# Kernel optimization log

Hardware: AMD Instinct MI355X
Metric: run time of the kernel (lower is better)

Reference implementation:

```python
import jax, jax.numpy as jnp
import numpy as np

B, T, EMB, H = 8, 1024, 128, 8


def setup_inputs() -> dict:
    key = jax.random.key(0)
    ks = jax.random.split(key, 7)
    s = 0.02
    return {
        "x": jax.random.normal(ks[0], (B, T, EMB), dtype=jnp.float32),
        "mask": jax.random.randint(ks[1], (1, T, T), 0, 2, dtype=jnp.int32),
        "Wk": (jax.random.normal(ks[2], (EMB * H, EMB), dtype=jnp.float32) * s),
        "Wq": (jax.random.normal(ks[3], (EMB * H, EMB), dtype=jnp.float32) * s),
        "Wv": (jax.random.normal(ks[4], (EMB * H, EMB), dtype=jnp.float32) * s),
        "Wu": (jax.random.normal(ks[5], (EMB, EMB * H), dtype=jnp.float32) * s),
        "bu": (jax.random.normal(ks[6], (EMB,), dtype=jnp.float32) * s),
    }


def reference(x, mask, Wk, Wq, Wv, Wu, bu):
    b, t, e = x.shape  # e == emb; per-head dim also == emb in this module
    h = Wk.shape[0] // e
    # projections: (b,t,e) @ (e, h*e) -> (b,t,h,e) -> (b,h,t,e)
    q = (x @ Wq.T).reshape(b, t, h, e).transpose(0, 2, 1, 3)
    k = (x @ Wk.T).reshape(b, t, h, e).transpose(0, 2, 1, 3)
    v = (x @ Wv.T).reshape(b, t, h, e).transpose(0, 2, 1, 3)
    scale = e ** 0.25  # torch scales q and k each by e**(1/4)
    dot = jnp.einsum('bhqe,bhke->bhqk', q / scale, k / scale)
    # causal mask: strictly-upper triangle (offset=1) set to -inf FIRST
    causal = jnp.triu(jnp.ones((t, t), dtype=bool), k=1)
    dot = jnp.where(causal, -jnp.inf, dot)
    # padding mask: where mask==0 set to -1e9 (overwrites -inf where overlapping)
    dot = jnp.where(mask[:, None] == 0, jnp.float32(-1e9), dot)
    attn = jax.nn.softmax(dot, axis=-1)
    out = jnp.einsum('bhqk,bhke->bhqe', attn, v)
    out = out.transpose(0, 2, 1, 3).reshape(b, t, h * e)
    return out @ Wu.T + bu
```

## Files before the change

### kernel.cpp

```cpp
#include <hip/hip_runtime.h>

#define Bn 8
#define Hn 8
#define Tn 1024
#define Dn 128

typedef __attribute__((ext_vector_type(8))) short bf16x8;
typedef __attribute__((ext_vector_type(4))) float f32x4;

typedef __attribute__((address_space(3))) unsigned int lds_as_t;
typedef __attribute__((address_space(1))) const unsigned int glb_as_t;

static __device__ __forceinline__ void gload_lds16(const unsigned short* g, unsigned short* l) {
    __builtin_amdgcn_global_load_lds((glb_as_t*)g, (lds_as_t*)l, 16, 0, 0);
}
static __device__ __forceinline__ void gload_lds16b(const char* g, char* l) {
    __builtin_amdgcn_global_load_lds((glb_as_t*)g, (lds_as_t*)l, 16, 0, 0);
}

static __device__ __forceinline__ unsigned short f2bf(float f) {
    union { float f; unsigned int u; } v; v.f = f;
    unsigned int u = v.u;
    return (unsigned short)((u + 0x7FFFu + ((u >> 16) & 1u)) >> 16);
}
static __device__ __forceinline__ int pack_bf16_trunc(float lo, float hi) {
    union { float f; unsigned int u; } a, b;
    a.f = lo; b.f = hi;
    return (int)__builtin_amdgcn_perm(b.u, a.u, 0x07060302u);
}

__global__ __launch_bounds__(256) void prep_kernel(
    const float* __restrict__ x,  const float* __restrict__ Wq,
    const float* __restrict__ Wk, const float* __restrict__ Wv,
    const float* __restrict__ Wu, const int* __restrict__ mask,
    const float* __restrict__ bu, float* __restrict__ outp,
    unsigned short* __restrict__ xb,  unsigned short* __restrict__ wqB,
    unsigned short* __restrict__ wkB, unsigned short* __restrict__ wvB,
    unsigned short* __restrict__ wuF, unsigned long long* __restrict__ bits)
{
    const int blk = blockIdx.x;
    const int tid = threadIdx.x;

    if (blk < 1408) {
        const float* in; unsigned short* out; int i4;
        if (blk < 1024)      { in = x;  out = xb;  i4 = blk * 256 + tid; }
        else if (blk < 1152) { in = Wq; out = wqB; i4 = (blk - 1024) * 256 + tid; }
        else if (blk < 1280) { in = Wk; out = wkB; i4 = (blk - 1152) * 256 + tid; }
        else                 { in = Wv; out = wvB; i4 = (blk - 1280) * 256 + tid; }
        float4 f = ((const float4*)in)[i4];
        ushort4 o;
        o.x = f2bf(f.x); o.y = f2bf(f.y); o.z = f2bf(f.z); o.w = f2bf(f.w);
        int base = i4 * 4;
        int row = base >> 7, col = base & 127;
        int scol = (((col >> 3) ^ (row & 15)) << 3) | (col & 7);
        *(ushort4*)(out + row * 128 + scol) = o;
    } else if (blk < 1536) {
        if (tid < 128) {
            int id = (blk - 1408) * 128 + tid;
            int lane_ = id & 63;
            int fid = id >> 6;
            int nt = fid & 7, ks = (fid >> 3) & 3, h = fid >> 5;
            int row = nt * 16 + (lane_ & 15);
            int col = h * 128 + ks * 32 + (lane_ >> 4) * 8;
            const float* src = Wu + (size_t)row * 1024 + col;
            float4 f0 = *(const float4*)(src);
            float4 f1 = *(const float4*)(src + 4);
            unsigned short o[8];
            o[0] = f2bf(f0.x); o[1] = f2bf(f0.y); o[2] = f2bf(f0.z); o[3] = f2bf(f0.w);
            o[4] = f2bf(f1.x); o[5] = f2bf(f1.y); o[6] = f2bf(f1.z); o[7] = f2bf(f1.w);
            *(ushort4*)(wuF + (size_t)id * 8)     = *(ushort4*)&o[0];
            *(ushort4*)(wuF + (size_t)id * 8 + 4) = *(ushort4*)&o[4];
        }
    } else if (blk < 2560) {
        int wid  = (blk - 1536) * 4 + (tid >> 6);
        int lane = tid & 63;
#pragma unroll
        for (int i = 0; i < 4; i++) {
            int widx = wid * 4 + i;
            int row = widx >> 4, kt = widx & 15;
            int v = mask[row * Tn + kt * 64 + lane];
            unsigned long long b = __ballot(v != 0);
            if (lane == 0) bits[kt * Tn + row] = b;
        }
    } else {
        int f4 = (blk - 2560) * 1024 + tid * 4;
#pragma unroll
        for (int i = 0; i < 4; i++)
            ((float4*)outp)[f4 + i] = ((const float4*)bu)[(f4 + i) & 31];
    }
}

__global__ __launch_bounds__(256, 1) void qkv_kernel(
    const unsigned short* __restrict__ xb,
    const unsigned short* __restrict__ wqB,
    const unsigned short* __restrict__ wkB,
    const unsigned short* __restrict__ wvB,
    char* __restrict__ Q,
    char* __restrict__ K,
    unsigned short* __restrict__ Vt)
{
    const int bx = blockIdx.x, by = blockIdx.y;
    const int wave = threadIdx.x >> 6;
    const int lane = threadIdx.x & 63;
    const int l16  = lane & 15;
    const int quad = lane >> 4;
    const int wm = wave & 1, wn = wave >> 1;

    __shared__ __align__(16) unsigned short As[128 * 128];
    __shared__ __align__(16) unsigned short Bs[3][128 * 128];
    __shared__ __align__(16) char escr[128 * 144];

    const unsigned short* Ag = xb + (size_t)bx * 128 * 128;
    const unsigned short* Bg0 = wqB + (size_t)by * 128 * 128;
    const unsigned short* Bg1 = wkB + (size_t)by * 128 * 128;
    const unsigned short* Bg2 = wvB + (size_t)by * 128 * 128;

#pragma unroll
    for (int i = 0; i < 8; i++) {
        int base = (wave * 8 + i) * 512;
        gload_lds16(Ag  + base + lane * 8, &As[base]);
        gload_lds16(Bg0 + base + lane * 8, &Bs[0][base]);
    }
    __syncthreads();

    bf16x8 a[4][4];
#pragma unroll
    for (int mt = 0; mt < 4; mt++) {
        int row = wm * 64 + mt * 16 + l16;
#pragma unroll
        for (int ks = 0; ks < 4; ks++)
            a[mt][ks] = *(const bf16x8*)(&As[row * 128 + (((ks * 4 + quad) ^ (row & 15)) << 3)]);
    }

    const int h_ = by;
    const int b_ = bx >> 3;
    f32x4 acc[4][4];

    {
#pragma unroll
        for (int i = 0; i < 8; i++) {
            int base = (wave * 8 + i) * 512;
            gload_lds16(Bg1 + base + lane * 8, &Bs[1][base]);
        }
#pragma unroll
        for (int nt = 0; nt < 4; nt++) {
            int row = wn * 64 + nt * 16 + l16;
            bf16x8 b4[4];
#pragma unroll
            for (int ks = 0; ks < 4; ks++)
                b4[ks] = *(const bf16x8*)(&Bs[0][row * 128 + (((ks * 4 + quad) ^ (row & 15)) << 3)]);
#pragma unroll
            for (int mt = 0; mt < 4; mt++) {
                f32x4 c = {0.f, 0.f, 0.f, 0.f};
#pragma unroll
                for (int ks = 0; ks < 4; ks++)
                    c = __builtin_amdgcn_mfma_f32_16x16x32_bf16(a[mt][ks], b4[ks], c, 0, 0, 0);
                acc[mt][nt] = c;
            }
        }
#pragma unroll
        for (int mt = 0; mt < 4; mt++) {
#pragma unroll
            for (int nt = 0; nt < 4; nt++) {
                int w = __builtin_amdgcn_cvt_pk_fp8_f32(acc[mt][nt][0], acc[mt][nt][1], 0, false);
                w = __builtin_amdgcn_cvt_pk_fp8_f32(acc[mt][nt][2], acc[mt][nt][3], w, true);
                int col = wn * 64 + nt * 16 + l16;
#pragma unroll
                for (int r = 0; r < 4; r++)
                    escr[(wm * 64 + mt * 16 + quad * 4 + r) * 144 + col] = (char)(w >> (8 * r));
            }
        }
        __syncthreads();
        const int f = threadIdx.x;
        int row = f >> 1;
        int t_in = (bx & 7) * 128 + row;
        size_t rowbase = ((size_t)((b_ * Hn + h_) * Tn + t_in)) * 128;
#pragma unroll
        for (int i = 0; i < 4; i++) {
            int c = (f & 1) * 4 + i;
            int4 v = *(const int4*)(escr + row * 144 + c * 16);
            *(int4*)(Q + rowbase + c * 16) = v;
        }
    }

    {
#pragma unroll
        for (int i = 0; i < 8; i++) {
            int base = (wave * 8 + i) * 512;
            gload_lds16(Bg2 + base + lane * 8, &Bs[2][base]);
        }
#pragma unroll
        for (int nt = 0; nt < 4; nt++) {
            int row = wn * 64 + nt * 16 + l16;
            bf16x8 b4[4];
#pragma unroll
            for (int ks = 0; ks < 4; ks++)
                b4[ks] = *(const bf16x8*)(&Bs[1][row * 128 + (((ks * 4 + quad) ^ (row & 15)) << 3)]);
#pragma unroll
            for (int mt = 0; mt < 4; mt++) {
                f32x4 c = {0.f, 0.f, 0.f, 0.f};
#pragma unroll
                for (int ks = 0; ks < 4; ks++)
                    c = __builtin_amdgcn_mfma_f32_16x16x32_bf16(a[mt][ks], b4[ks], c, 0, 0, 0);
                acc[mt][nt] = c;
            }
        }
        __syncthreads();
#pragma unroll
        for (int mt = 0; mt < 4; mt++) {
#pragma unroll
            for (int nt = 0; nt < 4; nt++) {
                int w = __builtin_amdgcn_cvt_pk_fp8_f32(acc[mt][nt][0], acc[mt][nt][1], 0, false);
                w = __builtin_amdgcn_cvt_pk_fp8_f32(acc[mt][nt][2], acc[mt][nt][3], w, true);
                int col = wn * 64 + nt * 16 + l16;
#pragma unroll
                for (int r = 0; r < 4; r++)
                    escr[(wm * 64 + mt * 16 + quad * 4 + r) * 144 + col] = (char)(w >> (8 * r));
            }
        }
        __syncthreads();
        const int f = threadIdx.x;
        int row = f >> 1;
        int t_in = (bx & 7) * 128 + row;
        size_t rowbase = ((size_t)((b_ * Hn + h_) * Tn + t_in)) * 128;
#pragma unroll
        for (int i = 0; i < 4; i++) {
            int c = (f & 1) * 4 + i;
            int4 v = *(const int4*)(escr + row * 144 + c * 16);
            int cc = c ^ (row & 7);
            *(int4*)(K + rowbase + cc * 16) = v;
        }
    }

    {
#pragma unroll
        for (int nt = 0; nt < 4; nt++) {
            int row = wn * 64 + nt * 16 + l16;
            bf16x8 b4[4];
#pragma unroll
            for (int ks = 0; ks < 4; ks++)
                b4[ks] = *(const bf16x8*)(&Bs[2][row * 128 + (((ks * 4 + quad) ^ (row & 15)) << 3)]);
#pragma unroll
            for (int mt = 0; mt < 4; mt++) {
                f32x4 c = {0.f, 0.f, 0.f, 0.f};
#pragma unroll
                for (int ks = 0; ks < 4; ks++)
                    c = __builtin_amdgcn_mfma_f32_16x16x32_bf16(a[mt][ks], b4[ks], c, 0, 0, 0);
                acc[mt][nt] = c;
            }
        }
#pragma unroll
        for (int mt = 0; mt < 4; mt++) {
            int m_base = bx * 128 + wm * 64 + mt * 16 + quad * 4;
            int t0 = m_base & 1023;
#pragma unroll
            for (int nt = 0; nt < 4; nt++) {
                int e_ = wn * 64 + nt * 16 + l16;
                int kt_ = t0 >> 6, tc0 = t0 & 63;
                size_t off = ((((size_t)(b_ * Hn + h_) * 16 + kt_) * 128 + e_) << 6)
                           + ((((tc0 >> 3) ^ (e_ & 7)) << 3) | (tc0 & 7));
                ushort4 v4;
                v4.x = f2bf(acc[mt][nt][0]); v4.y = f2bf(acc[mt][nt][1]);
                v4.z = f2bf(acc[mt][nt][2]); v4.w = f2bf(acc[mt][nt][3]);
                *(ushort4*)(Vt + off) = v4;
            }
        }
    }
}

__global__ __launch_bounds__(256, 3) void attn_kernel(
    const char* __restrict__ Q,
    const char* __restrict__ K,
    const unsigned short* __restrict__ Vt,
    const unsigned long long* __restrict__ mbits,
    const unsigned short* __restrict__ wuF,
    float* __restrict__ out)
{
    const int qt   = 15 - ((blockIdx.x + blockIdx.y) & 15);
    const int bh   = blockIdx.y;
    const int wave = threadIdx.x >> 6;
    const int lane = threadIdx.x & 63;
    const int l16  = lane & 15;
    const int quad = lane >> 4;

    __shared__ __align__(16) char kbuf[2][64 * 128];
    __shared__ __align__(16) unsigned short vbuf[2][128 * 64];

    const char* Qb = Q  + (size_t)bh * Tn * Dn;
    const char* Kb = K  + (size_t)bh * Tn * Dn;
    const unsigned short* Vb = Vt + (size_t)bh * (16 * 128 * 64);

    const int q0 = qt * 64 + wave * 16;
    const int qrow = q0 + quad * 4;

    long qf[4];
#pragma unroll
    for (int ks = 0; ks < 4; ks++)
        qf[ks] = *(const long*)(Qb + (size_t)(q0 + l16) * 128 + ks * 32 + quad * 8);

    bf16x8 ones;
#pragma unroll
    for (int j = 0; j < 8; j++) ones[j] = (short)0x3F80;

    f32x4 o[8];
#pragma unroll
    for (int et = 0; et < 8; et++) o[et] = (f32x4){0.f, 0.f, 0.f, 0.f};
    f32x4 lacc = {0.f, 0.f, 0.f, 0.f};

    const float SL = 0.12752041570284543f;

    const int idx0 = (l16 << 2) + ((quad & 1) << 7);
    const int idx1 = idx0 + 64;
    const bool hiQ = (quad >> 1) != 0;

#pragma unroll
    for (int i = 0; i < 2; i++) {
        int base = (wave * 2 + i) * 1024;
        gload_lds16b(Kb + base + lane * 16, &kbuf[0][base]);
    }
#pragma unroll
    for (int i = 0; i < 4; i++) {
        int base = (wave * 4 + i) * 512;
        gload_lds16(Vb + base + lane * 8, &vbuf[0][base]);
    }

    for (int kt = 0; kt <= qt; kt++) {
        const int cur = kt & 1;
        __syncthreads();

        if (kt < qt) {
            const char* Kg = Kb + (kt + 1) * (64 * 128);
            const unsigned short* Vg = Vb + (kt + 1) * (128 * 64);
#pragma unroll
            for (int i = 0; i < 2; i++) {
                int base = (wave * 2 + i) * 1024;
                gload_lds16b(Kg + base + lane * 16, &kbuf[cur ^ 1][base]);
            }
#pragma unroll
            for (int i = 0; i < 4; i++) {
                int base = (wave * 4 + i) * 512;
                gload_lds16(Vg + base + lane * 8, &vbuf[cur ^ 1][base]);
            }
        }

        const unsigned long long mw = mbits[kt * Tn + q0 + l16];

        f32x4 s[4];
#pragma unroll
        for (int nt = 0; nt < 4; nt++) {
            int row = nt * 16 + l16;
            long a4[4];
#pragma unroll
            for (int ks = 0; ks < 4; ks++) {
                int c = ks * 2 + (quad >> 1);
                a4[ks] = *(const long*)(&kbuf[cur][row * 128 + (((c ^ (row & 7)) << 4) | ((quad & 1) << 3))]);
            }
            f32x4 c = {0.f, 0.f, 0.f, 0.f};
#pragma unroll
            for (int ks = 0; ks < 4; ks++)
                c = __builtin_amdgcn_mfma_f32_16x16x32_fp8_fp8(a4[ks], qf[ks], c, 0, 0, 0);
            s[nt] = c;
        }

        const int kc0 = kt * 64;
        const int qglob = q0 + l16;
        int w[4][2];
#pragma unroll
        for (int nt = 0; nt < 4; nt++) {
            float pv[4];
#pragma unroll
            for (int r = 0; r < 4; r++) {
                int bit = nt * 16 + quad * 4 + r;
                bool live = ((mw >> bit) & 1ULL) && (kc0 + bit <= qglob);
                pv[r] = live ? __builtin_amdgcn_exp2f(s[nt][r] * SL) : 0.f;
            }
            w[nt][0] = pack_bf16_trunc(pv[0], pv[1]);
            w[nt][1] = pack_bf16_trunc(pv[2], pv[3]);
        }

        bf16x8 pf[2];
#pragma unroll
        for (int k2 = 0; k2 < 2; k2++) {
            union { int i[4]; bf16x8 v; } u;
#pragma unroll
            for (int d = 0; d < 4; d++) {
                int idx = (d < 2) ? idx0 : idx1;
                int va = __builtin_amdgcn_ds_bpermute(idx, w[2 * k2][d & 1]);
                int vb = __builtin_amdgcn_ds_bpermute(idx, w[2 * k2 + 1][d & 1]);
                u.i[d] = hiQ ? vb : va;
            }
            pf[k2] = u.v;
        }

#pragma unroll
        for (int k2 = 0; k2 < 2; k2++)
            lacc = __builtin_amdgcn_mfma_f32_16x16x32_bf16(pf[k2], ones, lacc, 0, 0, 0);

#pragma unroll
        for (int et = 0; et < 8; et++) {
            int row = et * 16 + l16;
#pragma unroll
            for (int k2 = 0; k2 < 2; k2++) {
                bf16x8 b = *(const bf16x8*)(&vbuf[cur][row * 64 + (((k2 * 4 + quad) ^ (l16 & 7)) << 3)]);
                o[et] = __builtin_amdgcn_mfma_f32_16x16x32_bf16(pf[k2], b, o[et], 0, 0, 0);
            }
        }
    }

    __syncthreads();
    {
        bool deg = (lacc[0] == 0.f) | (lacc[1] == 0.f) | (lacc[2] == 0.f) | (lacc[3] == 0.f);
        if (__ballot(deg) != 0ULL) {
            unsigned short* pb = (unsigned short*)((char*)kbuf + wave * 2304);
            unsigned short dsel[4];
#pragma unroll
            for (int r = 0; r < 4; r++) dsel[r] = (lacc[r] == 0.f) ? (unsigned short)0x3F80 : (unsigned short)0;
            for (int kt = 0; kt < 16; kt++) {
                unsigned long long mw2[4];
#pragma unroll
                for (int r = 0; r < 4; r++) mw2[r] = mbits[kt * Tn + qrow + r];
#pragma unroll
                for (int nt = 0; nt < 4; nt++) {
                    int bi = nt * 16 + l16;
#pragma unroll
                    for (int r = 0; r < 4; r++)
                        pb[(quad * 4 + r) * 72 + bi] = ((mw2[r] >> bi) & 1ULL) ? (unsigned short)0 : dsel[r];
                }
                bf16x8 pf[2];
#pragma unroll
                for (int k2 = 0; k2 < 2; k2++)
                    pf[k2] = *(const bf16x8*)(&pb[l16 * 72 + k2 * 32 + quad * 8]);
#pragma unroll
                for (int k2 = 0; k2 < 2; k2++)
                    lacc = __builtin_amdgcn_mfma_f32_16x16x32_bf16(pf[k2], ones, lacc, 0, 0, 0);
                const unsigned short* Vg = Vb + kt * (128 * 64);
#pragma unroll
                for (int et = 0; et < 8; et++) {
#pragma unroll
                    for (int k2 = 0; k2 < 2; k2++) {
                        bf16x8 b = *(const bf16x8*)(Vg + (et * 16 + l16) * 64 + (((k2 * 4 + quad) ^ (l16 & 7)) << 3));
                        o[et] = __builtin_amdgcn_mfma_f32_16x16x32_bf16(pf[k2], b, o[et], 0, 0, 0);
                    }
                }
            }
        }
    }

    const int b_ = bh >> 3, h_ = bh & 7;
    {
        unsigned short* tile = (unsigned short*)((char*)vbuf + wave * 4608);
#pragma unroll
        for (int r = 0; r < 4; r++) {
            float inv = 1.f / lacc[r];
            int row = quad * 4 + r;
#pragma unroll
            for (int et = 0; et < 8; et++)
                tile[row * 144 + et * 16 + l16] = f2bf(o[et][r] * inv);
        }

        bf16x8 a4[4];
#pragma unroll
        for (int ks = 0; ks < 4; ks++)
            a4[ks] = *(const bf16x8*)(&tile[l16 * 144 + ks * 32 + quad * 8]);

        const unsigned short* wf = wuF + (size_t)h_ * (4 * 8 * 64 * 8);
        f32x4 acc2[8];
#pragma unroll
        for (int nt = 0; nt < 8; nt++) acc2[nt] = (f32x4){0.f, 0.f, 0.f, 0.f};
#pragma unroll
        for (int ks = 0; ks < 4; ks++) {
#pragma unroll
            for (int nt = 0; nt < 8; nt++) {
                bf16x8 b = *(const bf16x8*)(wf + ((size_t)(ks * 8 + nt) * 64 + lane) * 8);
                acc2[nt] = __builtin_amdgcn_mfma_f32_16x16x32_bf16(a4[ks], b, acc2[nt], 0, 0, 0);
            }
        }

#pragma unroll
        for (int nt = 0; nt < 8; nt++) {
            int n = nt * 16 + l16;
#pragma unroll
            for (int r = 0; r < 4; r++) {
                int q = q0 + quad * 4 + r;
                atomicAdd(&out[(size_t)(b_ * Tn + q) * Dn + n], acc2[nt][r]);
            }
        }
    }
}

extern "C" void kernel_launch(void* const* d_in, const int* in_sizes, int n_in,
                              void* d_out, int out_size, void* d_ws, size_t ws_size,
                              hipStream_t stream) {
    const float* x   = (const float*)d_in[0];
    const int* mask  = (const int*)d_in[1];
    const float* Wk  = (const float*)d_in[2];
    const float* Wq  = (const float*)d_in[3];
    const float* Wv  = (const float*)d_in[4];
    const float* Wu  = (const float*)d_in[5];
    const float* bu  = (const float*)d_in[6];
    float* out = (float*)d_out;

    char* ws = (char*)d_ws;
    unsigned short* xb  = (unsigned short*)ws; ws += (size_t)8192 * 128 * 2;
    unsigned short* wqB = (unsigned short*)ws; ws += (size_t)1024 * 128 * 2;
    unsigned short* wkB = (unsigned short*)ws; ws += (size_t)1024 * 128 * 2;
    unsigned short* wvB = (unsigned short*)ws; ws += (size_t)1024 * 128 * 2;
    unsigned short* wuF = (unsigned short*)ws; ws += (size_t)128 * 1024 * 2;
    char* Qf  = ws; ws += (size_t)64 * 1024 * 128;
    char* Kf  = ws; ws += (size_t)64 * 1024 * 128;
    unsigned short* Vtw = (unsigned short*)ws; ws += (size_t)64 * 1024 * 128 * 2;
    unsigned long long* mb = (unsigned long long*)ws; ws += (size_t)1024 * 16 * 8;

    prep_kernel<<<dim3(2816), 256, 0, stream>>>(x, Wq, Wk, Wv, Wu, mask, bu, out,
                                                xb, wqB, wkB, wvB, wuF, mb);
    qkv_kernel<<<dim3(64, 8), 256, 0, stream>>>(xb, wqB, wkB, wvB, Qf, Kf, Vtw);
    attn_kernel<<<dim3(16, 64), 256, 0, stream>>>(Qf, Kf, Vtw, mb, wuF, out);
}
```

Measured before the change: 148.2 us.

## Process 128 queries per block with two 16-row subtiles per wave

Each wave now handles two 16-row query subtiles, so every K and V fragment loaded from LDS feeds twice as many MFMAs. The grid shrinks from 1024 to 512 blocks, and the query-block index is mirrored across the halves of the 1D grid to balance causal work. Waves whose rows end before the current key tile skip the compute. Register pressure roughly doubles for the accumulators, so launch bounds drop to 2 blocks per CU, which reduces occupancy and latency hiding.

```diff
diff --git a/kernel.cpp b/kernel.cpp
--- a/kernel.cpp
+++ b/kernel.cpp
@@ -268,7 +268,7 @@
     }
 }
 
-__global__ __launch_bounds__(256, 3) void attn_kernel(
+__global__ __launch_bounds__(256, 2) void attn_kernel(
     const char* __restrict__ Q,
     const char* __restrict__ K,
     const unsigned short* __restrict__ Vt,
@@ -276,8 +276,9 @@
     const unsigned short* __restrict__ wuF,
     float* __restrict__ out)
 {
-    const int qt   = 15 - ((blockIdx.x + blockIdx.y) & 15);
-    const int bh   = blockIdx.y;
+    const int id   = blockIdx.x;
+    const int qb   = (id & 7) ^ (7 * ((id >> 8) & 1));
+    const int bh   = (id >> 3) & 63;
     const int wave = threadIdx.x >> 6;
     const int lane = threadIdx.x & 63;
     const int l16  = lane & 15;
@@ -290,22 +291,30 @@
     const char* Kb = K  + (size_t)bh * Tn * Dn;
     const unsigned short* Vb = Vt + (size_t)bh * (16 * 128 * 64);
 
-    const int q0 = qt * 64 + wave * 16;
-    const int qrow = q0 + quad * 4;
-
-    long qf[4];
-#pragma unroll
-    for (int ks = 0; ks < 4; ks++)
-        qf[ks] = *(const long*)(Qb + (size_t)(q0 + l16) * 128 + ks * 32 + quad * 8);
+    const int blkkt = 2 * qb + 1;
+    const int q0w   = qb * 128 + wave * 32;
+    const int q0s[2] = { q0w, q0w + 16 };
+    const int wkmax = (q0w + 31) >> 6;
+
+    long qf[2][4];
+#pragma unroll
+    for (int st = 0; st < 2; st++)
+#pragma unroll
+        for (int ks = 0; ks < 4; ks++)
+            qf[st][ks] = *(const long*)(Qb + (size_t)(q0s[st] + l16) * 128 + ks * 32 + quad * 8);
 
     bf16x8 ones;
 #pragma unroll
     for (int j = 0; j < 8; j++) ones[j] = (short)0x3F80;
 
-    f32x4 o[8];
-#pragma unroll
-    for (int et = 0; et < 8; et++) o[et] = (f32x4){0.f, 0.f, 0.f, 0.f};
-    f32x4 lacc = {0.f, 0.f, 0.f, 0.f};
+    f32x4 o[2][8];
+#pragma unroll
+    for (int st = 0; st < 2; st++)
+#pragma unroll
+        for (int et = 0; et < 8; et++) o[st][et] = (f32x4){0.f, 0.f, 0.f, 0.f};
+    f32x4 lacc[2];
+    lacc[0] = (f32x4){0.f, 0.f, 0.f, 0.f};
+    lacc[1] = (f32x4){0.f, 0.f, 0.f, 0.f};
 
     const float SL = 0.12752041570284543f;
 
@@ -324,11 +333,11 @@
         gload_lds16(Vb + base + lane * 8, &vbuf[0][base]);
     }
 
-    for (int kt = 0; kt <= qt; kt++) {
+    for (int kt = 0; kt <= blkkt; kt++) {
         const int cur = kt & 1;
         __syncthreads();
 
-        if (kt < qt) {
+        if (kt < blkkt) {
             const char* Kg = Kb + (kt + 1) * (64 * 128);
             const unsigned short* Vg = Vb + (kt + 1) * (128 * 64);
 #pragma unroll
@@ -343,103 +352,126 @@
             }
         }
 
-        const unsigned long long mw = mbits[kt * Tn + q0 + l16];
-
-        f32x4 s[4];
-#pragma unroll
-        for (int nt = 0; nt < 4; nt++) {
-            int row = nt * 16 + l16;
-            long a4[4];
-#pragma unroll
-            for (int ks = 0; ks < 4; ks++) {
-                int c = ks * 2 + (quad >> 1);
-                a4[ks] = *(const long*)(&kbuf[cur][row * 128 + (((c ^ (row & 7)) << 4) | ((quad & 1) << 3))]);
-            }
-            f32x4 c = {0.f, 0.f, 0.f, 0.f};
-#pragma unroll
-            for (int ks = 0; ks < 4; ks++)
-                c = __builtin_amdgcn_mfma_f32_16x16x32_fp8_fp8(a4[ks], qf[ks], c, 0, 0, 0);
-            s[nt] = c;
-        }
-
-        const int kc0 = kt * 64;
-        const int qglob = q0 + l16;
-        int w[4][2];
-#pragma unroll
-        for (int nt = 0; nt < 4; nt++) {
-            float pv[4];
-#pragma unroll
-            for (int r = 0; r < 4; r++) {
-                int bit = nt * 16 + quad * 4 + r;
-                bool live = ((mw >> bit) & 1ULL) && (kc0 + bit <= qglob);
-                pv[r] = live ? __builtin_amdgcn_exp2f(s[nt][r] * SL) : 0.f;
-            }
-            w[nt][0] = pack_bf16_trunc(pv[0], pv[1]);
-            w[nt][1] = pack_bf16_trunc(pv[2], pv[3]);
-        }
-
-        bf16x8 pf[2];
-#pragma unroll
-        for (int k2 = 0; k2 < 2; k2++) {
-            union { int i[4]; bf16x8 v; } u;
-#pragma unroll
-            for (int d = 0; d < 4; d++) {
-                int idx = (d < 2) ? idx0 : idx1;
-                int va = __builtin_amdgcn_ds_bpermute(idx, w[2 * k2][d & 1]);
-                int vb = __builtin_amdgcn_ds_bpermute(idx, w[2 * k2 + 1][d & 1]);
-                u.i[d] = hiQ ? vb : va;
-            }
-            pf[k2] = u.v;
-        }
-
-#pragma unroll
-        for (int k2 = 0; k2 < 2; k2++)
-            lacc = __builtin_amdgcn_mfma_f32_16x16x32_bf16(pf[k2], ones, lacc, 0, 0, 0);
-
-#pragma unroll
-        for (int et = 0; et < 8; et++) {
-            int row = et * 16 + l16;
-#pragma unroll
-            for (int k2 = 0; k2 < 2; k2++) {
-                bf16x8 b = *(const bf16x8*)(&vbuf[cur][row * 64 + (((k2 * 4 + quad) ^ (l16 & 7)) << 3)]);
-                o[et] = __builtin_amdgcn_mfma_f32_16x16x32_bf16(pf[k2], b, o[et], 0, 0, 0);
+        if (kt <= wkmax) {
+            unsigned long long mw[2];
+            mw[0] = mbits[kt * Tn + q0s[0] + l16];
+            mw[1] = mbits[kt * Tn + q0s[1] + l16];
+
+            f32x4 s[2][4];
+#pragma unroll
+            for (int nt = 0; nt < 4; nt++) {
+                int row = nt * 16 + l16;
+                long a4[4];
+#pragma unroll
+                for (int ks = 0; ks < 4; ks++) {
+                    int c = ks * 2 + (quad >> 1);
+                    a4[ks] = *(const long*)(&kbuf[cur][row * 128 + (((c ^ (row & 7)) << 4) | ((quad & 1) << 3))]);
+                }
+#pragma unroll
+                for (int st = 0; st < 2; st++) {
+                    f32x4 c = {0.f, 0.f, 0.f, 0.f};
+#pragma unroll
+                    for (int ks = 0; ks < 4; ks++)
+                        c = __builtin_amdgcn_mfma_f32_16x16x32_fp8_fp8(a4[ks], qf[st][ks], c, 0, 0, 0);
+                    s[st][nt] = c;
+                }
+            }
+
+            const int kc0 = kt * 64;
+            bf16x8 pf[2][2];
+#pragma unroll
+            for (int st = 0; st < 2; st++) {
+                const int qglob = q0s[st] + l16;
+                int w[4][2];
+#pragma unroll
+                for (int nt = 0; nt < 4; nt++) {
+                    float pv[4];
+#pragma unroll
+                    for (int r = 0; r < 4; r++) {
+                        int bit = nt * 16 + quad * 4 + r;
+                        bool live = ((mw[st] >> bit) & 1ULL) && (kc0 + bit <= qglob);
+                        pv[r] = live ? __builtin_amdgcn_exp2f(s[st][nt][r] * SL) : 0.f;
+                    }
+                    w[nt][0] = pack_bf16_trunc(pv[0], pv[1]);
+                    w[nt][1] = pack_bf16_trunc(pv[2], pv[3]);
+                }
+#pragma unroll
+                for (int k2 = 0; k2 < 2; k2++) {
+                    union { int i[4]; bf16x8 v; } u;
+#pragma unroll
+                    for (int d = 0; d < 4; d++) {
+                        int idx = (d < 2) ? idx0 : idx1;
+                        int va = __builtin_amdgcn_ds_bpermute(idx, w[2 * k2][d & 1]);
+                        int vb = __builtin_amdgcn_ds_bpermute(idx, w[2 * k2 + 1][d & 1]);
+                        u.i[d] = hiQ ? vb : va;
+                    }
+                    pf[st][k2] = u.v;
+                }
+            }
+
+#pragma unroll
+            for (int st = 0; st < 2; st++)
+#pragma unroll
+                for (int k2 = 0; k2 < 2; k2++)
+                    lacc[st] = __builtin_amdgcn_mfma_f32_16x16x32_bf16(pf[st][k2], ones, lacc[st], 0, 0, 0);
+
+#pragma unroll
+            for (int et = 0; et < 8; et++) {
+                int row = et * 16 + l16;
+#pragma unroll
+                for (int k2 = 0; k2 < 2; k2++) {
+                    bf16x8 b = *(const bf16x8*)(&vbuf[cur][row * 64 + (((k2 * 4 + quad) ^ (l16 & 7)) << 3)]);
+                    o[0][et] = __builtin_amdgcn_mfma_f32_16x16x32_bf16(pf[0][k2], b, o[0][et], 0, 0, 0);
+                    o[1][et] = __builtin_amdgcn_mfma_f32_16x16x32_bf16(pf[1][k2], b, o[1][et], 0, 0, 0);
+                }
             }
         }
     }
 
     __syncthreads();
     {
-        bool deg = (lacc[0] == 0.f) | (lacc[1] == 0.f) | (lacc[2] == 0.f) | (lacc[3] == 0.f);
+        bool deg = false;
+#pragma unroll
+        for (int st = 0; st < 2; st++)
+#pragma unroll
+            for (int r = 0; r < 4; r++) deg |= (lacc[st][r] == 0.f);
         if (__ballot(deg) != 0ULL) {
             unsigned short* pb = (unsigned short*)((char*)kbuf + wave * 2304);
-            unsigned short dsel[4];
-#pragma unroll
-            for (int r = 0; r < 4; r++) dsel[r] = (lacc[r] == 0.f) ? (unsigned short)0x3F80 : (unsigned short)0;
+            unsigned short dsel[2][4];
+#pragma unroll
+            for (int st = 0; st < 2; st++)
+#pragma unroll
+                for (int r = 0; r < 4; r++)
+                    dsel[st][r] = (lacc[st][r] == 0.f) ? (unsigned short)0x3F80 : (unsigned short)0;
             for (int kt = 0; kt < 16; kt++) {
-                unsigned long long mw2[4];
-#pragma unroll
-                for (int r = 0; r < 4; r++) mw2[r] = mbits[kt * Tn + qrow + r];
-#pragma unroll
-                for (int nt = 0; nt < 4; nt++) {
-                    int bi = nt * 16 + l16;
-#pragma unroll
-                    for (int r = 0; r < 4; r++)
-                        pb[(quad * 4 + r) * 72 + bi] = ((mw2[r] >> bi) & 1ULL) ? (unsigned short)0 : dsel[r];
-                }
-                bf16x8 pf[2];
-#pragma unroll
-                for (int k2 = 0; k2 < 2; k2++)
-                    pf[k2] = *(const bf16x8*)(&pb[l16 * 72 + k2 * 32 + quad * 8]);
-#pragma unroll
-                for (int k2 = 0; k2 < 2; k2++)
-                    lacc = __builtin_amdgcn_mfma_f32_16x16x32_bf16(pf[k2], ones, lacc, 0, 0, 0);
-                const unsigned short* Vg = Vb + kt * (128 * 64);
-#pragma unroll
-                for (int et = 0; et < 8; et++) {
-#pragma unroll
-                    for (int k2 = 0; k2 < 2; k2++) {
-                        bf16x8 b = *(const bf16x8*)(Vg + (et * 16 + l16) * 64 + (((k2 * 4 + quad) ^ (l16 & 7)) << 3));
-                        o[et] = __builtin_amdgcn_mfma_f32_16x16x32_bf16(pf[k2], b, o[et], 0, 0, 0);
+#pragma unroll
+                for (int st = 0; st < 2; st++) {
+                    int qrow = q0s[st] + quad * 4;
+                    unsigned long long mw2[4];
+#pragma unroll
+                    for (int r = 0; r < 4; r++) mw2[r] = mbits[kt * Tn + qrow + r];
+#pragma unroll
+                    for (int nt = 0; nt < 4; nt++) {
+                        int bi = nt * 16 + l16;
+#pragma unroll
+                        for (int r = 0; r < 4; r++)
+                            pb[(quad * 4 + r) * 72 + bi] = ((mw2[r] >> bi) & 1ULL) ? (unsigned short)0 : dsel[st][r];
+                    }
+                    bf16x8 pf[2];
+#pragma unroll
+                    for (int k2 = 0; k2 < 2; k2++)
+                        pf[k2] = *(const bf16x8*)(&pb[l16 * 72 + k2 * 32 + quad * 8]);
+#pragma unroll
+                    for (int k2 = 0; k2 < 2; k2++)
+                        lacc[st] = __builtin_amdgcn_mfma_f32_16x16x32_bf16(pf[k2], ones, lacc[st], 0, 0, 0);
+                    const unsigned short* Vg = Vb + kt * (128 * 64);
+#pragma unroll
+                    for (int et = 0; et < 8; et++) {
+#pragma unroll
+                        for (int k2 = 0; k2 < 2; k2++) {
+                            bf16x8 b = *(const bf16x8*)(Vg + (et * 16 + l16) * 64 + (((k2 * 4 + quad) ^ (l16 & 7)) << 3));
+                            o[st][et] = __builtin_amdgcn_mfma_f32_16x16x32_bf16(pf[k2], b, o[st][et], 0, 0, 0);
+                        }
                     }
                 }
             }
@@ -447,15 +479,17 @@
     }
 
     const int b_ = bh >> 3, h_ = bh & 7;
-    {
+    const unsigned short* wf = wuF + (size_t)h_ * (4 * 8 * 64 * 8);
+#pragma unroll
+    for (int st = 0; st < 2; st++) {
         unsigned short* tile = (unsigned short*)((char*)vbuf + wave * 4608);
 #pragma unroll
         for (int r = 0; r < 4; r++) {
-            float inv = 1.f / lacc[r];
+            float inv = 1.f / lacc[st][r];
             int row = quad * 4 + r;
 #pragma unroll
             for (int et = 0; et < 8; et++)
-                tile[row * 144 + et * 16 + l16] = f2bf(o[et][r] * inv);
+                tile[row * 144 + et * 16 + l16] = f2bf(o[st][et][r] * inv);
         }
 
         bf16x8 a4[4];
@@ -463,7 +497,6 @@
         for (int ks = 0; ks < 4; ks++)
             a4[ks] = *(const bf16x8*)(&tile[l16 * 144 + ks * 32 + quad * 8]);
 
-        const unsigned short* wf = wuF + (size_t)h_ * (4 * 8 * 64 * 8);
         f32x4 acc2[8];
 #pragma unroll
         for (int nt = 0; nt < 8; nt++) acc2[nt] = (f32x4){0.f, 0.f, 0.f, 0.f};
@@ -481,7 +514,7 @@
             int n = nt * 16 + l16;
 #pragma unroll
             for (int r = 0; r < 4; r++) {
-                int q = q0 + quad * 4 + r;
+                int q = q0s[st] + quad * 4 + r;
                 atomicAdd(&out[(size_t)(b_ * Tn + q) * Dn + n], acc2[nt][r]);
             }
         }
@@ -514,5 +547,5 @@
     prep_kernel<<<dim3(2816), 256, 0, stream>>>(x, Wq, Wk, Wv, Wu, mask, bu, out,
                                                 xb, wqB, wkB, wvB, wuF, mb);
     qkv_kernel<<<dim3(64, 8), 256, 0, stream>>>(xb, wqB, wkB, wvB, Qf, Kf, Vtw);
-    attn_kernel<<<dim3(16, 64), 256, 0, stream>>>(Qf, Kf, Vtw, mb, wuF, out);
-}
+    attn_kernel<<<dim3(512), 256, 0, stream>>>(Qf, Kf, Vtw, mb, wuF, out);
+}
```

New measurement: 147.7 us. About the same (-0.3%).
